# Performance work log

Measured on AMD Instinct MI355X. Metric: run time of the kernel, lower is better.

The kernel has to match this reference:

```python
import jax, jax.numpy as jnp
import numpy as np

B, H, S, D = 512, 1024, 1024, 128
TOPK = 32

def setup_inputs() -> dict:
    key = jax.random.key(0)
    ks = jax.random.split(key, 12)
    w = lambda k, shape: (jax.random.normal(k, shape, dtype=jnp.float32) * 0.02)
    return {
        "latent": jax.random.normal(ks[0], (B, H), dtype=jnp.float32),
        "memory": jax.random.normal(ks[1], (B, S, D), dtype=jnp.float32),
        "read_query_w": w(ks[2], (H, D)),
        "read_query_b": jnp.zeros((D,), jnp.float32),
        "memory_key": w(ks[3], (S, D)),
        "write_gate_w": w(ks[4], (H + D, 1)),
        "write_gate_b": jnp.zeros((1,), jnp.float32),
        "dmd_proj_w": w(ks[5], (H + D, 1)),
        "dmd_proj_b": jnp.zeros((1,), jnp.float32),
        "phase_proj_w": w(ks[6], (H, 1)),
        "phase_proj_b": jnp.zeros((1,), jnp.float32),
        "write_value_w": w(ks[7], (H, D)),
        "write_value_b": jnp.zeros((D,), jnp.float32),
    }

def reference(latent, memory, read_query_w, read_query_b, memory_key,
              write_gate_w, write_gate_b, dmd_proj_w, dmd_proj_b,
              phase_proj_w, phase_proj_b, write_value_w, write_value_b):
    # soft read over memory slots
    query = latent @ read_query_w + read_query_b              # [B, D]
    logits = jnp.einsum('bd,sd->bs', query, memory_key)       # [B, S]
    weights = jax.nn.softmax(logits, axis=-1)
    # top-k masked renormalization (topk=32 < S)
    _, topk_idx = jax.lax.top_k(weights, TOPK)                # [B, K]
    rows = jnp.arange(weights.shape[0])[:, None]
    mask = jnp.zeros_like(weights).at[rows, topk_idx].set(1.0)
    weights = weights * mask
    weights = weights / jnp.clip(weights.sum(-1, keepdims=True), 1e-8)
    read = jnp.einsum('bs,bsd->bd', weights, memory)          # [B, D]
    gate_input = jnp.concatenate([latent, read], axis=-1)     # [B, H+D]
    # sigmoid gate (gating_mode='sigmoid')
    gate = jax.nn.sigmoid(gate_input @ write_gate_w + write_gate_b)  # [B, 1]
    # dmd gating
    dmd_signal = jnp.tanh(gate_input @ dmd_proj_w + dmd_proj_b)
    gate = jnp.clip(gate * (0.75 + 0.5 * (dmd_signal + 1.0) * 0.5), 0.0, 1.0)
    # phase gating
    phase = latent @ phase_proj_w + phase_proj_b
    gate = gate * (0.5 * (1.0 + jnp.cos(phase)))
    # soft scatter-write update
    value = (latent @ write_value_w + write_value_b)[:, None, :]      # [B, 1, D]
    gw = gate[:, :, None] * weights[:, :, None]                       # [B, S, 1]
    new_memory = (1.0 - gw) * memory + gw * value                     # [B, S, D]
    return read, new_memory, weights
```

## Files before the change

kernel.cpp:

```cpp
#include <hip/hip_runtime.h>
#include <math.h>

#define NB 512
#define NH 1024
#define NS 1024
#define ND 128
#define NK 32

typedef float fx4 __attribute__((ext_vector_type(4)));

__device__ __forceinline__ void bar_lgkm() {
  asm volatile("s_waitcnt lgkmcnt(0)" ::: "memory");
  __builtin_amdgcn_s_barrier();
}
__device__ __forceinline__ void bar_full() {
  asm volatile("s_waitcnt vmcnt(0) lgkmcnt(0)" ::: "memory");
  __builtin_amdgcn_s_barrier();
}

__global__ __launch_bounds__(512, 4) void fused_kernel(
    const float* __restrict__ latent,
    const float* __restrict__ memory,
    const float* __restrict__ rq_w,
    const float* __restrict__ rq_b,
    const float* __restrict__ mem_key,
    const float* __restrict__ wg_w,
    const float* __restrict__ wg_b,
    const float* __restrict__ dmd_w,
    const float* __restrict__ dmd_b,
    const float* __restrict__ ph_w,
    const float* __restrict__ ph_b,
    const float* __restrict__ wv_w,
    const float* __restrict__ wv_b,
    float* __restrict__ out_read,
    float* __restrict__ out_mem,
    float* __restrict__ out_wts)
{
  const int b    = blockIdx.x;
  const int tid  = threadIdx.x;
  const int lane = tid & 63;
  const int wv   = tid >> 6;

  __shared__ __align__(16) float lat[NH];
  __shared__ __align__(16) float wfull[NS];
  __shared__ __align__(16) fx4   part4[512];
  __shared__ __align__(16) float qv[ND];
  __shared__ float rd[ND];
  __shared__ float tvw[256];
  __shared__ int   tiw[256];
  __shared__ float wkL[NK];
  __shared__ int   tiL[NK];
  __shared__ __align__(16) float valw_s[ND];
  __shared__ float gred[24];
  __shared__ float scal[1];

  float* part4f = (float*)part4;

  const fx4* __restrict__ msrc = (const fx4*)memory + (size_t)b * (NS * ND / 4);
  fx4*       __restrict__ mdst = (fx4*)out_mem      + (size_t)b * (NS * ND / 4);
  fx4 bufA[8], bufB[8];
  int cur_l = 0, cur_s = 0;

#define CK_LOAD(BUF, N)  { _Pragma("unroll") \
    for (int j = 0; j < (N); ++j) \
      BUF[j] = __builtin_nontemporal_load(msrc + (size_t)(cur_l + j) * 512 + tid); \
    cur_l += (N); }
#define CK_STORE(BUF, N) { _Pragma("unroll") \
    for (int j = 0; j < (N); ++j) \
      __builtin_nontemporal_store(BUF[j], mdst + (size_t)(cur_s + j) * 512 + tid); \
    cur_s += (N); }

  const int og = tid & 31;
  const int pp = tid >> 5;
  const fx4* lat4 = (const fx4*)lat;

  CK_LOAD(bufA, 8);
  if (tid < 256)
    ((fx4*)lat)[tid] = ((const fx4*)(latent + (size_t)b * NH))[tid];
  bar_lgkm();

  CK_LOAD(bufB, 4);
  CK_STORE(bufA, 8);
  {
    const fx4* W4 = (const fx4*)rq_w;
    fx4 acc = {0.f, 0.f, 0.f, 0.f};
    const int hbase = pp * 64;
    #pragma unroll 4
    for (int j = 0; j < 16; ++j) {
      fx4 l4 = lat4[(hbase >> 2) + j];
      acc += l4.x * W4[(size_t)(hbase + 4*j    ) * 32 + og];
      acc += l4.y * W4[(size_t)(hbase + 4*j + 1) * 32 + og];
      acc += l4.z * W4[(size_t)(hbase + 4*j + 2) * 32 + og];
      acc += l4.w * W4[(size_t)(hbase + 4*j + 3) * 32 + og];
    }
    part4[pp * 32 + og] = acc;
  }
  bar_lgkm();

  CK_LOAD(bufA, 8);
  CK_STORE(bufB, 4);
  if (tid < ND) {
    float q = rq_b[tid];
    #pragma unroll
    for (int p = 0; p < 16; ++p) q += part4f[p * 128 + tid];
    qv[tid] = q;
  }
  bar_lgkm();

  CK_LOAD(bufB, 8);
  CK_STORE(bufA, 8);
  float r0 = 0.f, r1 = 0.f;
  {
    const float4* q4 = (const float4*)qv;
    const float4* k0 = (const float4*)(mem_key + (size_t)tid * ND);
    const float4* k1 = (const float4*)(mem_key + (size_t)(tid + 512) * ND);
    #pragma unroll 8
    for (int i = 0; i < ND / 4; ++i) {
      float4 q = q4[i];
      float4 x = k0[i];
      float4 y = k1[i];
      r0 += q.x * x.x + q.y * x.y + q.z * x.z + q.w * x.w;
      r1 += q.x * y.x + q.y * y.y + q.z * y.z + q.w * y.w;
    }
  }
  const float NEGINF = -3.0e38f;
  float selv = NEGINF; int seli = -1; float wkreg = 0.f;
  {
    const int s0 = tid, s1 = tid + 512;
    float v0 = r0, v1 = r1;
    for (int kk = 0; kk < NK; ++kk) {
      float best; int bi;
      if (v0 >= v1) { best = v0; bi = s0; } else { best = v1; bi = s1; }
      #pragma unroll
      for (int off = 1; off < 64; off <<= 1) {
        float ov = __shfl_xor(best, off);
        int   oi = __shfl_xor(bi, off);
        if (ov > best || (ov == best && oi < bi)) { best = ov; bi = oi; }
      }
      if (lane == 0) { tvw[(wv << 5) + kk] = best; tiw[(wv << 5) + kk] = bi; }
      if (bi == s0) v0 = NEGINF;
      if (bi == s1) v1 = NEGINF;
    }
  }
  wfull[tid] = 0.f; wfull[tid + 512] = 0.f;
  bar_lgkm();

  CK_LOAD(bufA, 8);
  CK_STORE(bufB, 8);
  if (wv == 0) {
    float m0 = tvw[lane], m1 = tvw[lane + 64], m2 = tvw[lane + 128], m3 = tvw[lane + 192];
    int   i0 = tiw[lane], i1 = tiw[lane + 64], i2 = tiw[lane + 128], i3 = tiw[lane + 192];
    for (int kk = 0; kk < NK; ++kk) {
      float best = m0; int bi = i0;
      if (m1 > best || (m1 == best && i1 < bi)) { best = m1; bi = i1; }
      if (m2 > best || (m2 == best && i2 < bi)) { best = m2; bi = i2; }
      if (m3 > best || (m3 == best && i3 < bi)) { best = m3; bi = i3; }
      #pragma unroll
      for (int off = 1; off < 64; off <<= 1) {
        float ov = __shfl_xor(best, off);
        int   oi = __shfl_xor(bi, off);
        if (ov > best || (ov == best && oi < bi)) { best = ov; bi = oi; }
      }
      if (kk == lane) { selv = best; seli = bi; }
      if (bi == i0) m0 = NEGINF;
      if (bi == i1) m1 = NEGINF;
      if (bi == i2) m2 = NEGINF;
      if (bi == i3) m3 = NEGINF;
    }
    float maxv = __shfl(selv, 0);
    float e = (lane < NK) ? expf(selv - maxv) : 0.f;
    float s = e;
    #pragma unroll
    for (int off = 1; off < 64; off <<= 1) s += __shfl_xor(s, off);
    wkreg = e / s;
    if (lane < NK) { wkL[lane] = wkreg; tiL[lane] = seli; }
  }
  bar_lgkm();

  CK_LOAD(bufB, 4);
  CK_STORE(bufA, 8);
  if (wv == 0 && lane < NK) wfull[seli] = wkreg;
  {
    const fx4* mb4 = (const fx4*)(memory + (size_t)b * NS * ND);
    const int k0i = pp, k1i = pp + 16;
    fx4 racc = wkL[k0i] * mb4[(size_t)tiL[k0i] * 32 + og]
             + wkL[k1i] * mb4[(size_t)tiL[k1i] * 32 + og];
    part4[pp * 32 + og] = racc;
  }
  bar_lgkm();

  CK_LOAD(bufA, 8);
  CK_STORE(bufB, 4);
  if (tid < ND) {
    float r = 0.f;
    #pragma unroll
    for (int p = 0; p < 16; ++p) r += part4f[p * 128 + tid];
    rd[tid] = r;
    out_read[(size_t)b * ND + tid] = r;
  }
  bar_lgkm();

  CK_LOAD(bufB, 4);
  CK_STORE(bufA, 8);
  {
    float p1 = 0.f, p2 = 0.f, p3 = 0.f;
    if (tid < 256) {
      fx4 l4 = lat4[tid];
      fx4 a = ((const fx4*)wg_w)[tid];
      fx4 d4 = ((const fx4*)dmd_w)[tid];
      fx4 c4 = ((const fx4*)ph_w)[tid];
      p1 = l4.x*a.x + l4.y*a.y + l4.z*a.z + l4.w*a.w;
      p2 = l4.x*d4.x + l4.y*d4.y + l4.z*d4.z + l4.w*d4.w;
      p3 = l4.x*c4.x + l4.y*c4.y + l4.z*c4.z + l4.w*c4.w;
    } else if (tid < 384) {
      const int d = tid - 256;
      float r = rd[d];
      p1 = r * wg_w[NH + d];
      p2 = r * dmd_w[NH + d];
    }
    #pragma unroll
    for (int off = 1; off < 64; off <<= 1) {
      p1 += __shfl_xor(p1, off);
      p2 += __shfl_xor(p2, off);
      p3 += __shfl_xor(p3, off);
    }
    if (lane == 0) { gred[wv] = p1; gred[8 + wv] = p2; gred[16 + wv] = p3; }
  }
  {
    const fx4* W4 = (const fx4*)wv_w;
    fx4 acc = {0.f, 0.f, 0.f, 0.f};
    const int hbase = pp * 64;
    #pragma unroll 4
    for (int j = 0; j < 16; ++j) {
      fx4 l4 = lat4[(hbase >> 2) + j];
      acc += l4.x * W4[(size_t)(hbase + 4*j    ) * 32 + og];
      acc += l4.y * W4[(size_t)(hbase + 4*j + 1) * 32 + og];
      acc += l4.z * W4[(size_t)(hbase + 4*j + 2) * 32 + og];
      acc += l4.w * W4[(size_t)(hbase + 4*j + 3) * 32 + og];
    }
    part4[pp * 32 + og] = acc;
  }
  bar_lgkm();

  CK_LOAD(bufA, 6);
  CK_STORE(bufB, 4);
  if (tid == 0) {
    float z1 = wg_b[0], z2 = dmd_b[0], z3 = ph_b[0];
    #pragma unroll
    for (int k = 0; k < 8; ++k) { z1 += gred[k]; z2 += gred[8 + k]; z3 += gred[16 + k]; }
    float g  = 1.f / (1.f + expf(-z1));
    float dm = tanhf(z2);
    g = g * (0.75f + 0.25f * (dm + 1.f));
    g = fminf(fmaxf(g, 0.f), 1.f);
    g = g * (0.5f * (1.f + cosf(z3)));
    scal[0] = g;
  }
  bar_lgkm();

  CK_LOAD(bufB, 6);
  CK_STORE(bufA, 6);
  if (tid < 256)
    ((fx4*)(out_wts + (size_t)b * NS))[tid] = ((const fx4*)wfull)[tid];
  if (tid < ND) {
    float v = wv_b[tid];
    #pragma unroll
    for (int p = 0; p < 16; ++p) v += part4f[p * 128 + tid];
    valw_s[tid] = v;
  }
  bar_lgkm();

  CK_STORE(bufB, 6);
  bar_full();
  {
    const float g = scal[0];
    const fx4* v4 = (const fx4*)valw_s;
    #pragma unroll
    for (int u = 0; u < 2; ++u) {
      const int idx = tid + u * 512;
      const int k   = idx >> 5;
      const int c   = idx & 31;
      const float w = g * wkL[k];
      const int row = tiL[k];
      const fx4 m = msrc[(size_t)row * 32 + c];
      __builtin_nontemporal_store((1.f - w) * m + w * v4[c],
                                  mdst + (size_t)row * 32 + c);
    }
  }
#undef CK_LOAD
#undef CK_STORE
}

extern "C" void kernel_launch(void* const* d_in, const int* in_sizes, int n_in,
                              void* d_out, int out_size, void* d_ws, size_t ws_size,
                              hipStream_t stream) {
  const float* latent  = (const float*)d_in[0];
  const float* memory  = (const float*)d_in[1];
  const float* rq_w    = (const float*)d_in[2];
  const float* rq_b    = (const float*)d_in[3];
  const float* mem_key = (const float*)d_in[4];
  const float* wg_w    = (const float*)d_in[5];
  const float* wg_b    = (const float*)d_in[6];
  const float* dmd_w   = (const float*)d_in[7];
  const float* dmd_b   = (const float*)d_in[8];
  const float* ph_w    = (const float*)d_in[9];
  const float* ph_b    = (const float*)d_in[10];
  const float* wv_w    = (const float*)d_in[11];
  const float* wv_b    = (const float*)d_in[12];

  float* out_read = (float*)d_out;
  float* out_mem  = out_read + (size_t)NB * ND;
  float* out_wts  = out_mem + (size_t)NB * NS * ND;

  fused_kernel<<<NB, 512, 0, stream>>>(
      latent, memory, rq_w, rq_b, mem_key, wg_w, wg_b, dmd_w, dmd_b,
      ph_w, ph_b, wv_w, wv_b, out_read, out_mem, out_wts);
}
```

Baseline: 507.1 us.

## Split bulk memory copy into separate copy blocks and a fixup kernel

The bulk copy of memory to new_memory is no longer interleaved with the per-batch compute phases. Instead, 2048 extra blocks in the same grid do a plain streaming copy, and the compute blocks write gate weights, indices and values to workspace. A second kernel then rewrites the 32 selected rows per batch. This decouples the bandwidth-bound copy from the latency-bound compute and drops the hand-placed waitcnt barriers. In exchange it adds a second launch and re-reads and rewrites the top-k rows, and it relies on stream ordering to avoid a race between the copy and the fixup.

```diff
diff --git a/kernel.cpp b/kernel.cpp
--- a/kernel.cpp
+++ b/kernel.cpp
@@ -7,18 +7,12 @@
 #define ND 128
 #define NK 32
 
+#define NCOPY 2048
+#define NGRID (NB + NCOPY)
+
 typedef float fx4 __attribute__((ext_vector_type(4)));
 
-__device__ __forceinline__ void bar_lgkm() {
-  asm volatile("s_waitcnt lgkmcnt(0)" ::: "memory");
-  __builtin_amdgcn_s_barrier();
-}
-__device__ __forceinline__ void bar_full() {
-  asm volatile("s_waitcnt vmcnt(0) lgkmcnt(0)" ::: "memory");
-  __builtin_amdgcn_s_barrier();
-}
-
-__global__ __launch_bounds__(512, 4) void fused_kernel(
+__global__ __launch_bounds__(512) void fused_kernel(
     const float* __restrict__ latent,
     const float* __restrict__ memory,
     const float* __restrict__ rq_w,
@@ -34,10 +28,30 @@
     const float* __restrict__ wv_b,
     float* __restrict__ out_read,
     float* __restrict__ out_mem,
-    float* __restrict__ out_wts)
+    float* __restrict__ out_wts,
+    float* __restrict__ gwk,
+    int*   __restrict__ idxw,
+    float* __restrict__ valw)
 {
-  const int b    = blockIdx.x;
-  const int tid  = threadIdx.x;
+  const int bid = blockIdx.x;
+  const int tid = threadIdx.x;
+
+  if (bid >= NB) {
+    const size_t T   = (size_t)(bid - NB) * 512 + tid;
+    const size_t STR = (size_t)NCOPY * 512;
+    const fx4* __restrict__ src = (const fx4*)memory;
+    fx4*       __restrict__ dst = (fx4*)out_mem;
+    fx4 v[16];
+    #pragma unroll
+    for (int j = 0; j < 16; ++j)
+      v[j] = __builtin_nontemporal_load(src + T + (size_t)j * STR);
+    #pragma unroll
+    for (int j = 0; j < 16; ++j)
+      __builtin_nontemporal_store(v[j], dst + T + (size_t)j * STR);
+    return;
+  }
+
+  const int b    = bid;
   const int lane = tid & 63;
   const int wv   = tid >> 6;
 
@@ -50,37 +64,18 @@
   __shared__ int   tiw[256];
   __shared__ float wkL[NK];
   __shared__ int   tiL[NK];
-  __shared__ __align__(16) float valw_s[ND];
   __shared__ float gred[24];
   __shared__ float scal[1];
 
   float* part4f = (float*)part4;
-
-  const fx4* __restrict__ msrc = (const fx4*)memory + (size_t)b * (NS * ND / 4);
-  fx4*       __restrict__ mdst = (fx4*)out_mem      + (size_t)b * (NS * ND / 4);
-  fx4 bufA[8], bufB[8];
-  int cur_l = 0, cur_s = 0;
-
-#define CK_LOAD(BUF, N)  { _Pragma("unroll") \
-    for (int j = 0; j < (N); ++j) \
-      BUF[j] = __builtin_nontemporal_load(msrc + (size_t)(cur_l + j) * 512 + tid); \
-    cur_l += (N); }
-#define CK_STORE(BUF, N) { _Pragma("unroll") \
-    for (int j = 0; j < (N); ++j) \
-      __builtin_nontemporal_store(BUF[j], mdst + (size_t)(cur_s + j) * 512 + tid); \
-    cur_s += (N); }
-
   const int og = tid & 31;
   const int pp = tid >> 5;
   const fx4* lat4 = (const fx4*)lat;
 
-  CK_LOAD(bufA, 8);
   if (tid < 256)
     ((fx4*)lat)[tid] = ((const fx4*)(latent + (size_t)b * NH))[tid];
-  bar_lgkm();
-
-  CK_LOAD(bufB, 4);
-  CK_STORE(bufA, 8);
+  __syncthreads();
+
   {
     const fx4* W4 = (const fx4*)rq_w;
     fx4 acc = {0.f, 0.f, 0.f, 0.f};
@@ -95,20 +90,16 @@
     }
     part4[pp * 32 + og] = acc;
   }
-  bar_lgkm();
-
-  CK_LOAD(bufA, 8);
-  CK_STORE(bufB, 4);
+  __syncthreads();
+
   if (tid < ND) {
     float q = rq_b[tid];
     #pragma unroll
     for (int p = 0; p < 16; ++p) q += part4f[p * 128 + tid];
     qv[tid] = q;
   }
-  bar_lgkm();
-
-  CK_LOAD(bufB, 8);
-  CK_STORE(bufA, 8);
+  __syncthreads();
+
   float r0 = 0.f, r1 = 0.f;
   {
     const float4* q4 = (const float4*)qv;
@@ -143,10 +134,8 @@
     }
   }
   wfull[tid] = 0.f; wfull[tid + 512] = 0.f;
-  bar_lgkm();
-
-  CK_LOAD(bufA, 8);
-  CK_STORE(bufB, 8);
+  __syncthreads();
+
   if (wv == 0) {
     float m0 = tvw[lane], m1 = tvw[lane + 64], m2 = tvw[lane + 128], m3 = tvw[lane + 192];
     int   i0 = tiw[lane], i1 = tiw[lane + 64], i2 = tiw[lane + 128], i3 = tiw[lane + 192];
@@ -175,10 +164,8 @@
     wkreg = e / s;
     if (lane < NK) { wkL[lane] = wkreg; tiL[lane] = seli; }
   }
-  bar_lgkm();
-
-  CK_LOAD(bufB, 4);
-  CK_STORE(bufA, 8);
+  __syncthreads();
+
   if (wv == 0 && lane < NK) wfull[seli] = wkreg;
   {
     const fx4* mb4 = (const fx4*)(memory + (size_t)b * NS * ND);
@@ -187,10 +174,8 @@
              + wkL[k1i] * mb4[(size_t)tiL[k1i] * 32 + og];
     part4[pp * 32 + og] = racc;
   }
-  bar_lgkm();
-
-  CK_LOAD(bufA, 8);
-  CK_STORE(bufB, 4);
+  __syncthreads();
+
   if (tid < ND) {
     float r = 0.f;
     #pragma unroll
@@ -198,15 +183,13 @@
     rd[tid] = r;
     out_read[(size_t)b * ND + tid] = r;
   }
-  bar_lgkm();
-
-  CK_LOAD(bufB, 4);
-  CK_STORE(bufA, 8);
+  __syncthreads();
+
   {
     float p1 = 0.f, p2 = 0.f, p3 = 0.f;
     if (tid < 256) {
       fx4 l4 = lat4[tid];
-      fx4 a = ((const fx4*)wg_w)[tid];
+      fx4 a  = ((const fx4*)wg_w)[tid];
       fx4 d4 = ((const fx4*)dmd_w)[tid];
       fx4 c4 = ((const fx4*)ph_w)[tid];
       p1 = l4.x*a.x + l4.y*a.y + l4.z*a.z + l4.w*a.w;
@@ -240,10 +223,8 @@
     }
     part4[pp * 32 + og] = acc;
   }
-  bar_lgkm();
-
-  CK_LOAD(bufA, 6);
-  CK_STORE(bufB, 4);
+  __syncthreads();
+
   if (tid == 0) {
     float z1 = wg_b[0], z2 = dmd_b[0], z3 = ph_b[0];
     #pragma unroll
@@ -255,39 +236,49 @@
     g = g * (0.5f * (1.f + cosf(z3)));
     scal[0] = g;
   }
-  bar_lgkm();
-
-  CK_LOAD(bufB, 6);
-  CK_STORE(bufA, 6);
+  __syncthreads();
+
   if (tid < 256)
     ((fx4*)(out_wts + (size_t)b * NS))[tid] = ((const fx4*)wfull)[tid];
   if (tid < ND) {
     float v = wv_b[tid];
     #pragma unroll
     for (int p = 0; p < 16; ++p) v += part4f[p * 128 + tid];
-    valw_s[tid] = v;
-  }
-  bar_lgkm();
-
-  CK_STORE(bufB, 6);
-  bar_full();
-  {
-    const float g = scal[0];
-    const fx4* v4 = (const fx4*)valw_s;
-    #pragma unroll
-    for (int u = 0; u < 2; ++u) {
-      const int idx = tid + u * 512;
-      const int k   = idx >> 5;
-      const int c   = idx & 31;
-      const float w = g * wkL[k];
-      const int row = tiL[k];
-      const fx4 m = msrc[(size_t)row * 32 + c];
-      __builtin_nontemporal_store((1.f - w) * m + w * v4[c],
-                                  mdst + (size_t)row * 32 + c);
-    }
-  }
-#undef CK_LOAD
-#undef CK_STORE
+    valw[(size_t)b * ND + tid] = v;
+  }
+  if (tid < NK) {
+    gwk [(size_t)b * NK + tid] = scal[0] * wkL[tid];
+    idxw[(size_t)b * NK + tid] = tiL[tid];
+  }
+}
+
+__global__ __launch_bounds__(256) void fixup_kernel(
+    const float* __restrict__ memory,
+    const float* __restrict__ gwk,
+    const int*   __restrict__ idxw,
+    const float* __restrict__ valw,
+    float* __restrict__ out_mem)
+{
+  const int b = blockIdx.x, t = threadIdx.x;
+  __shared__ float w_s[NK];
+  __shared__ int   i_s[NK];
+  __shared__ __align__(16) float v_s[ND];
+  if (t < NK) { w_s[t] = gwk[(size_t)b * NK + t]; i_s[t] = idxw[(size_t)b * NK + t]; }
+  if (t < ND) v_s[t] = valw[(size_t)b * ND + t];
+  __syncthreads();
+  const fx4* __restrict__ mb = (const fx4*)(memory + (size_t)b * NS * ND);
+  fx4*       __restrict__ ob = (fx4*)(out_mem + (size_t)b * NS * ND);
+  const fx4* v4 = (const fx4*)v_s;
+  #pragma unroll
+  for (int u = 0; u < 4; ++u) {
+    const int e = t + u * 256;
+    const int k = e >> 5;
+    const int c = e & 31;
+    const float w = w_s[k];
+    const int row = i_s[k];
+    const fx4 m = mb[(size_t)row * 32 + c];
+    ob[(size_t)row * 32 + c] = (1.f - w) * m + w * v4[c];
+  }
 }
 
 extern "C" void kernel_launch(void* const* d_in, const int* in_sizes, int n_in,
@@ -311,7 +302,13 @@
   float* out_mem  = out_read + (size_t)NB * ND;
   float* out_wts  = out_mem + (size_t)NB * NS * ND;
 
-  fused_kernel<<<NB, 512, 0, stream>>>(
+  float* gwk  = (float*)d_ws;
+  int*   idxw = (int*)(gwk + (size_t)NB * NK);
+  float* valw = (float*)(idxw + (size_t)NB * NK);
+
+  fused_kernel<<<NGRID, 512, 0, stream>>>(
       latent, memory, rq_w, rq_b, mem_key, wg_w, wg_b, dmd_w, dmd_b,
-      ph_w, ph_b, wv_w, wv_b, out_read, out_mem, out_wts);
+      ph_w, ph_b, wv_w, wv_b, out_read, out_mem, out_wts, gwk, idxw, valw);
+
+  fixup_kernel<<<NB, 256, 0, stream>>>(memory, gwk, idxw, valw, out_mem);
 }
```

After: 622.8 us. 22.8% more time.
